# Kernel optimization log

Measured on AMD Instinct MI355X. Metric: run time of the kernel, lower is better.

Reference implementation:

```python
import jax, jax.numpy as jnp
import numpy as np

W_M = 1.0
SIGMA_BASE = 1.0
NUM_GROUPS = 2
NUM_CLASSES = 10
EPS = 1e-12
N, D = 4096, 512


def setup_inputs() -> dict:
    key = jax.random.key(0)
    k1, k2, k3, k4 = jax.random.split(key, 4)
    return {
        "f_s": jax.random.normal(k1, (N, D), dtype=jnp.float32),
        "f_t": jax.random.normal(k2, (N, D), dtype=jnp.float32),
        "groups": jax.random.randint(k3, (N,), 0, NUM_GROUPS),
        "labels": jax.random.randint(k4, (N,), 0, NUM_CLASSES),
    }


def _sqdist(e1, e2):
    # clamped squared euclidean pairwise distances [n1, n2]
    d = (jnp.sum(e1 * e1, axis=1)[:, None]
         + jnp.sum(e2 * e2, axis=1)[None, :]
         - 2.0 * (e1 @ e2.T))
    return jnp.maximum(d, EPS)


def reference(f_s, f_t, groups, labels):
    student = f_s.reshape(f_s.shape[0], -1)
    teacher = f_t.reshape(f_t.shape[0], -1)
    n = student.shape[0]

    D_TS = _sqdist(teacher, student)
    # sigma_avg computed under no_grad over the full teacher-vs-student pdist
    sigma_avg = jax.lax.stop_gradient(jnp.mean(D_TS))
    scale = 2.0 * SIGMA_BASE * sigma_avg

    K_TS = jnp.exp(-D_TS / scale)                      # [N, N]
    K_SS = jnp.exp(-_sqdist(student, student) / scale)  # [N, N]
    K_TT = jnp.exp(-_sqdist(teacher, teacher) / scale)  # [N, N]

    dt = student.dtype
    L = (labels[:, None] == jnp.arange(NUM_CLASSES)[None, :]).astype(dt)   # [N, C]
    Gm = (groups[:, None] == jnp.arange(NUM_GROUPS)[None, :]).astype(dt)   # [N, G]
    S = (L[:, :, None] * Gm[:, None, :]).reshape(n, NUM_CLASSES * NUM_GROUPS)  # [N, CG]

    n_t = L.sum(axis=0)                                 # [C]
    n_s = S.sum(axis=0).reshape(NUM_CLASSES, NUM_GROUPS)  # [C, G]

    # masked pair sums via two small matmuls each
    num_TT = jnp.einsum('nc,nc->c', L, K_TT @ L)                       # [C]
    num_SS = jnp.einsum('np,np->p', S, K_SS @ S).reshape(NUM_CLASSES, NUM_GROUPS)
    A_TS = (K_TS @ S).reshape(n, NUM_CLASSES, NUM_GROUPS)              # [N, C, G]
    num_TS = jnp.einsum('nc,ncg->cg', L, A_TS)                          # [C, G]

    safe_nt = jnp.maximum(n_t, 1.0)
    safe_ns = jnp.maximum(n_s, 1.0)
    mean_TT = num_TT / (safe_nt * safe_nt)              # [C]
    mean_SS = num_SS / (safe_ns * safe_ns)              # [C, G]
    mean_TS = num_TS / (safe_nt[:, None] * safe_ns)     # [C, G]

    valid = (n_t[:, None] > 0) & (n_s > 0)
    term = jnp.where(valid, mean_TT[:, None] + mean_SS - 2.0 * mean_TS, 0.0)
    return 0.5 * W_M * jnp.sum(term)
```

## Files before the change

kernel.cpp:

```cpp
#include <hip/hip_runtime.h>
#include <math.h>

#define NN 4096
#define DD 512
#define NC 10
#define NG 2

#define BM 128
#define BN 128
#define BK 32
#define NT (DD / BK)

#define TSLOT 512
#define SSLOT 256
#define TROWS (NC * TSLOT)
#define SROWS (NC * NG * SSLOT)
#define NTILES 320

typedef __bf16 bf16x8 __attribute__((ext_vector_type(8)));
typedef __bf16 bf16x4 __attribute__((ext_vector_type(4)));
typedef float f32x4 __attribute__((ext_vector_type(4)));

__device__ __forceinline__ void load_lds16(const __bf16* g, __bf16* l) {
    __builtin_amdgcn_global_load_lds((const __attribute__((address_space(1))) void*)g,
                                     (__attribute__((address_space(3))) void*)l, 16, 0, 0);
}

__global__ __launch_bounds__(1024) void k_sortcol(
    const int* __restrict__ labels, const int* __restrict__ groups,
    const float* __restrict__ ft, const float* __restrict__ fs,
    int* __restrict__ perm_t, int* __restrict__ perm_s,
    float* __restrict__ cnts, float* __restrict__ psum, float* __restrict__ ssq) {

    __shared__ int wtot[16][32];
    __shared__ int woff[16][32];
    __shared__ float redsq[4];

    int tid = threadIdx.x;

    if (blockIdx.x < 64) {
        if (tid >= 256) return;
        int b = blockIdx.x;
        int w = tid >> 6, lane = tid & 63;
        const float* srcm = (b < 32) ? ft : fs;
        int r0 = (b & 31) * 128;
        int c0 = tid, c1 = tid + 256;
        float a0 = 0.0f, a1 = 0.0f, sq = 0.0f;
        for (int rw = r0; rw < r0 + 128; ++rw) {
            float v0 = srcm[(size_t)rw * DD + c0];
            float v1 = srcm[(size_t)rw * DD + c1];
            a0 += v0; a1 += v1;
            sq += v0 * v0 + v1 * v1;
        }
        psum[(size_t)b * 512 + c0] = a0;
        psum[(size_t)b * 512 + c1] = a1;
#pragma unroll
        for (int o = 32; o; o >>= 1) sq += __shfl_xor(sq, o);
        if (lane == 0) redsq[w] = sq;
        __syncthreads();
        if (tid == 0) ssq[b] = redsq[0] + redsq[1] + redsq[2] + redsq[3];
        return;
    }

    int lane = tid & 63, w = tid >> 6;

    int4 lab = ((const int4*)labels)[tid];
    int4 grp = ((const int4*)groups)[tid];
    int l[4] = {lab.x, lab.y, lab.z, lab.w};
    int g[4] = {grp.x, grp.y, grp.z, grp.w};

    int cT[NC] = {}, cS[NC * NG] = {};
#pragma unroll
    for (int k = 0; k < 4; ++k) {
        int sb = 2 * l[k] + g[k];
#pragma unroll
        for (int c = 0; c < NC; ++c) cT[c] += (l[k] == c) ? 1 : 0;
#pragma unroll
        for (int c = 0; c < NC * NG; ++c) cS[c] += (sb == c) ? 1 : 0;
    }

    int eT[NC], eS[NC * NG];
#pragma unroll
    for (int c = 0; c < NC; ++c) {
        int x = cT[c];
#pragma unroll
        for (int o = 1; o < 64; o <<= 1) { int v = __shfl_up(x, o); if (lane >= o) x += v; }
        eT[c] = x - cT[c];
        if (lane == 63) wtot[w][c] = x;
    }
#pragma unroll
    for (int c = 0; c < NC * NG; ++c) {
        int x = cS[c];
#pragma unroll
        for (int o = 1; o < 64; o <<= 1) { int v = __shfl_up(x, o); if (lane >= o) x += v; }
        eS[c] = x - cS[c];
        if (lane == 63) wtot[w][NC + c] = x;
    }
    __syncthreads();

    if (tid < NC + NC * NG) {
        int run = 0;
        for (int ww = 0; ww < 16; ++ww) { woff[ww][tid] = run; run += wtot[ww][tid]; }
        int slot = (tid < NC) ? TSLOT : SSLOT;
        cnts[tid] = (float)((run < slot) ? run : slot);
    }
    __syncthreads();

    int runT[NC] = {}, runS[NC * NG] = {};
#pragma unroll
    for (int k = 0; k < 4; ++k) {
        int row = tid * 4 + k;
        int lb = l[k], sb = 2 * l[k] + g[k];
#pragma unroll
        for (int c = 0; c < NC; ++c)
            if (lb == c) {
                int rank = woff[w][c] + eT[c] + runT[c];
                if (rank < TSLOT) perm_t[c * TSLOT + rank] = row;
                runT[c]++;
            }
#pragma unroll
        for (int c = 0; c < NC * NG; ++c)
            if (sb == c) {
                int rank = woff[w][NC + c] + eS[c] + runS[c];
                if (rank < SSLOT) perm_s[c * SSLOT + rank] = row;
                runS[c]++;
            }
    }
}

__global__ void k_prep(const float* __restrict__ ft, const float* __restrict__ fs,
                       const int* __restrict__ perm_t, const int* __restrict__ perm_s,
                       __bf16* __restrict__ Tp, __bf16* __restrict__ Sp,
                       float* __restrict__ ntp, float* __restrict__ nsp,
                       const float* __restrict__ cnts,
                       const float* __restrict__ psum, const float* __restrict__ ssq,
                       float* __restrict__ gbkt, float* __restrict__ invscale) {
    int tid = threadIdx.x;
    if (blockIdx.x == 0 && tid < 64) gbkt[tid] = 0.0f;

    int w = tid >> 6, lane = tid & 63;
    int r = blockIdx.x * 4 + w;
    bool isT = r < TROWS;
    int rr = isT ? r : r - TROWS;
    int c  = isT ? (rr >> 9) : (rr >> 8);
    int j  = isT ? (rr & 511) : (rr & 255);
    int n  = (int)cnts[isT ? c : 10 + c];
    bool valid = j < n;
    int src = valid ? (isT ? perm_t[c * TSLOT + j] : perm_s[c * SSLOT + j]) : 0;
    const float* sp = (isT ? ft : fs) + (size_t)src * DD;
    __bf16* dp = (isT ? Tp : Sp) + (size_t)rr * DD;
    float s = 0.0f;
#pragma unroll
    for (int q = 0; q < 2; ++q) {
        float4 v;
        if (valid) v = ((const float4*)sp)[lane + 64 * q];
        else { v.x = 0.0f; v.y = 0.0f; v.z = 0.0f; v.w = 0.0f; }
        s += v.x * v.x + v.y * v.y + v.z * v.z + v.w * v.w;
        bf16x4 b4;
        b4[0] = (__bf16)v.x; b4[1] = (__bf16)v.y; b4[2] = (__bf16)v.z; b4[3] = (__bf16)v.w;
        *(bf16x4*)(dp + (lane + 64 * q) * 4) = b4;
    }
#pragma unroll
    for (int o = 32; o; o >>= 1) s += __shfl_xor(s, o);
    if (lane == 0) (isT ? ntp : nsp)[rr] = s;

    if (blockIdx.x != 1) return;
    __shared__ float red[8];
    float ssum = (tid < 64) ? ssq[tid] : 0.0f;
    float d = 0.0f;
    for (int col = tid; col < DD; col += 256) {
        float su = 0.0f, sv = 0.0f;
#pragma unroll
        for (int p = 0; p < 32; ++p) {
            su += psum[(size_t)p * 512 + col];
            sv += psum[(size_t)(p + 32) * 512 + col];
        }
        d += su * sv;
    }
#pragma unroll
    for (int o = 32; o; o >>= 1) { ssum += __shfl_xor(ssum, o); d += __shfl_xor(d, o); }
    if (lane == 0) { red[w] = ssum; red[w + 4] = d; }
    __syncthreads();
    if (tid == 0) {
        float S  = red[0] + red[1] + red[2] + red[3];
        float Dt = red[4] + red[5] + red[6] + red[7];
        float sigma = S / (float)NN - 2.0f * Dt / ((float)NN * (float)NN);
        invscale[0] = 1.0f / (2.0f * sigma);
    }
}

__global__ __launch_bounds__(256, 3) void k_gram_all(
    const __bf16* __restrict__ Tp, const __bf16* __restrict__ Sp,
    const float* __restrict__ ntp, const float* __restrict__ nsp,
    const float* __restrict__ cnts,
    const float* __restrict__ invscale_p, float* __restrict__ gbkt) {

    __shared__ __bf16 As[3][4 * 128 * 8];
    __shared__ __bf16 Bs[3][4 * 128 * 8];
    __shared__ float wred[4];

    int swz = ((int)blockIdx.x & 7) * 40 + ((int)blockIdx.x >> 3);
    int mode, bkt, diag, tiv, tjv;
    const __bf16 *A, *B;
    const float *nA, *nB;
    int nrow, ncol;

    if (swz < 100) {
        mode = 0;
        int c = swz / 10, k = swz % 10;
        int ti = 0;
        while (k >= 4 - ti) { k -= 4 - ti; ++ti; }
        int tj = ti + k;
        bkt = c; diag = (ti == tj); tiv = ti; tjv = tj;
        int rb = c * TSLOT + ti * 128, cb = c * TSLOT + tj * 128;
        A = Tp + (size_t)rb * DD; B = Tp + (size_t)cb * DD;
        nA = ntp + rb; nB = ntp + cb;
        int cntc = (int)cnts[c];
        nrow = cntc - ti * 128; ncol = cntc - tj * 128;
    } else if (swz < 160) {
        mode = 1;
        int q = swz - 100;
        int b = q / 3, k = q % 3;
        int ti = (k == 2) ? 1 : 0;
        int tj = (k == 0) ? 0 : 1;
        bkt = 10 + b; diag = (ti == tj); tiv = ti; tjv = tj;
        int rb = b * SSLOT + ti * 128, cb = b * SSLOT + tj * 128;
        A = Sp + (size_t)rb * DD; B = Sp + (size_t)cb * DD;
        nA = nsp + rb; nB = nsp + cb;
        int cntb = (int)cnts[10 + b];
        nrow = cntb - ti * 128; ncol = cntb - tj * 128;
    } else {
        mode = 2;
        int q = swz - 160;
        int c = q >> 4; q &= 15;
        int ti = q >> 2, sj = q & 3;
        int g = sj >> 1, st = sj & 1;
        bkt = 30 + 2 * c + g; diag = 0; tiv = 0; tjv = 0;
        int rb = c * TSLOT + ti * 128;
        int cb = (2 * c + g) * SSLOT + st * 128;
        A = Tp + (size_t)rb * DD; B = Sp + (size_t)cb * DD;
        nA = ntp + rb; nB = nsp + cb;
        nrow = (int)cnts[c] - ti * 128;
        ncol = (int)cnts[10 + 2 * c + g] - st * 128;
    }
    nrow = (nrow < 0) ? 0 : ((nrow > 128) ? 128 : nrow);
    ncol = (ncol < 0) ? 0 : ((ncol > 128) ? 128 : ncol);

    int tid = threadIdx.x;
    int lane = tid & 63, wid = tid >> 6;
    int wr = wid >> 1, wc = wid & 1;
    int l15 = lane & 15, l4 = lane >> 4;

    int ra = tid & 127;
    int qa = tid >> 7;
    const __bf16* gA = A + (size_t)ra * DD + qa * 8;
    const __bf16* gB = B + (size_t)ra * DD + qa * 8;

    f32x4 acc[4][4] = {};

#define STAGE(bb, tt)                                                          \
    do {                                                                       \
        int _k0 = (tt) * BK;                                                   \
        load_lds16(gA + _k0,      &As[(bb)][(size_t)tid * 8]);                 \
        load_lds16(gA + _k0 + 16, &As[(bb)][(size_t)(tid + 256) * 8]);         \
        load_lds16(gB + _k0,      &Bs[(bb)][(size_t)tid * 8]);                 \
        load_lds16(gB + _k0 + 16, &Bs[(bb)][(size_t)(tid + 256) * 8]);         \
    } while (0)

    STAGE(0, 0);
    STAGE(1, 1);
    asm volatile("s_waitcnt vmcnt(4)" ::: "memory");
    __builtin_amdgcn_s_barrier();
    __builtin_amdgcn_sched_barrier(0);

#pragma unroll
    for (int t = 0; t < NT; ++t) {
        int b = t % 3;
        bf16x8 af[4], bfr[4];
#pragma unroll
        for (int im = 0; im < 4; ++im)
            af[im] = *(const bf16x8*)&As[b][((size_t)l4 * 128 + wr * 64 + im * 16 + l15) * 8];
#pragma unroll
        for (int in = 0; in < 4; ++in)
            bfr[in] = *(const bf16x8*)&Bs[b][((size_t)l4 * 128 + wc * 64 + in * 16 + l15) * 8];
        if (t + 2 < NT) STAGE((t + 2) % 3, t + 2);
#pragma unroll
        for (int im = 0; im < 4; ++im)
#pragma unroll
            for (int in = 0; in < 4; ++in)
                acc[im][in] = __builtin_amdgcn_mfma_f32_16x16x32_bf16(af[im], bfr[in], acc[im][in], 0, 0, 0);
        if (t + 1 < NT) {
            if (t + 2 < NT) asm volatile("s_waitcnt vmcnt(4)" ::: "memory");
            else            asm volatile("s_waitcnt vmcnt(0)" ::: "memory");
            __builtin_amdgcn_s_barrier();
            __builtin_amdgcn_sched_barrier(0);
        }
    }
#undef STAGE

    float inv_scale = invscale_p[0];
    float nBv[4];
#pragma unroll
    for (int in = 0; in < 4; ++in)
        nBv[in] = nB[wc * 64 + in * 16 + l15];
    float ssum = 0.0f;
#pragma unroll
    for (int im = 0; im < 4; ++im) {
#pragma unroll
        for (int j = 0; j < 4; ++j) {
            int rl = wr * 64 + im * 16 + l4 * 4 + j;
            float ni = nA[rl];
#pragma unroll
            for (int in = 0; in < 4; ++in) {
                int cl_ = wc * 64 + in * 16 + l15;
                float d = ni + nBv[in] - 2.0f * acc[im][in][j];
                d = fmaxf(d, 1e-12f);
                float kv = __expf(-d * inv_scale);
                bool v = (rl < nrow) && (cl_ < ncol);
                if (mode == 2) {
                    ssum += v ? kv : 0.0f;
                } else {
                    int rg = tiv * 128 + rl, cg = tjv * 128 + cl_;
                    float wgt = !v ? 0.0f
                              : (diag ? (cg > rg ? 2.0f : (cg == rg ? 1.0f : 0.0f))
                                      : 2.0f);
                    ssum += wgt * kv;
                }
            }
        }
    }
#pragma unroll
    for (int o = 1; o < 64; o <<= 1) ssum += __shfl_xor(ssum, o);
    if (lane == 0) wred[wid] = ssum;
    __syncthreads();
    if (tid == 0) atomicAdd(&gbkt[bkt], wred[0] + wred[1] + wred[2] + wred[3]);
}

__global__ void k_out(const float* __restrict__ cnts, const float* __restrict__ gbkt,
                      float* __restrict__ out) {
    __shared__ float sh[80];
    int tid = threadIdx.x;
    if (tid < 30) sh[tid] = cnts[tid];
    else if (tid < 80) sh[tid] = gbkt[tid - 30];
    __syncthreads();
    if (tid == 0) {
        float total = 0.0f;
        for (int c = 0; c < NC; ++c) {
            float ntc = sh[c];
            float sn = fmaxf(ntc, 1.0f);
            float meanTT = sh[30 + c] / (sn * sn);
            for (int g = 0; g < NG; ++g) {
                float nsg = sh[10 + 2 * c + g];
                float ss = fmaxf(nsg, 1.0f);
                float meanSS = sh[40 + 2 * c + g] / (ss * ss);
                float meanTS = sh[60 + 2 * c + g] / (sn * ss);
                if (ntc > 0.0f && nsg > 0.0f)
                    total += meanTT + meanSS - 2.0f * meanTS;
            }
        }
        out[0] = 0.5f * total;
    }
}

extern "C" void kernel_launch(void* const* d_in, const int* in_sizes, int n_in,
                              void* d_out, int out_size, void* d_ws, size_t ws_size,
                              hipStream_t stream) {
    const float* fs     = (const float*)d_in[0];
    const float* ft     = (const float*)d_in[1];
    const int*   groups = (const int*)d_in[2];
    const int*   labels = (const int*)d_in[3];

    __bf16* Tp = (__bf16*)d_ws;
    __bf16* Sp = (__bf16*)d_ws + (size_t)TROWS * DD;
    float* wsf  = (float*)((char*)d_ws + (size_t)(TROWS + SROWS) * DD * sizeof(__bf16));
    float* ntp  = wsf;
    float* nsp  = wsf + 5120;
    float* gbkt = wsf + 10240;
    float* invs = wsf + 10304;
    float* ssq  = wsf + 10306;
    float* cnts = wsf + 10370;
    int* perm_t = (int*)(wsf + 10400);
    int* perm_s = (int*)(wsf + 15520);
    float* psum = wsf + 20640;

    k_sortcol<<<65, 1024, 0, stream>>>(labels, groups, ft, fs,
                                       perm_t, perm_s, cnts, psum, ssq);
    k_prep<<<2560, 256, 0, stream>>>(ft, fs, perm_t, perm_s, Tp, Sp, ntp, nsp,
                                     cnts, psum, ssq, gbkt, invs);
    k_gram_all<<<NTILES, 256, 0, stream>>>(Tp, Sp, ntp, nsp, cnts, invs, gbkt);
    k_out<<<1, 128, 0, stream>>>(cnts, gbkt, (float*)d_out);
}
```

Baseline: 60.04 us.

## Use 256x128 gram tiles with 512-thread blocks to cut tile count

Enlarges the gram-kernel tile from 128x128 to 256x128 using 8 waves per block, reducing the grid from 320 to 180 tiles. Each B tile is now reused across twice as many rows, and the tile enumeration for the symmetric TT/SS buckets is reworked, with the triangular weighting applied uniformly. The cost is that more upper-triangle work inside diagonal blocks is computed and discarded, and fewer blocks may leave compute units idle on a 256-CU part.

Measured after the change: 58.64 us. 1.02x faster.

```diff
diff --git a/kernel.cpp b/kernel.cpp
--- a/kernel.cpp
+++ b/kernel.cpp
@@ -6,7 +6,7 @@
 #define NC 10
 #define NG 2
 
-#define BM 128
+#define BM 256
 #define BN 128
 #define BK 32
 #define NT (DD / BK)
@@ -15,7 +15,7 @@
 #define SSLOT 256
 #define TROWS (NC * TSLOT)
 #define SROWS (NC * NG * SSLOT)
-#define NTILES 320
+#define NTILES 180
 
 typedef __bf16 bf16x8 __attribute__((ext_vector_type(8)));
 typedef __bf16 bf16x4 __attribute__((ext_vector_type(4)));
@@ -189,61 +189,60 @@
     }
 }
 
-__global__ __launch_bounds__(256, 3) void k_gram_all(
+__global__ __launch_bounds__(512, 2) void k_gram_all(
     const __bf16* __restrict__ Tp, const __bf16* __restrict__ Sp,
     const float* __restrict__ ntp, const float* __restrict__ nsp,
     const float* __restrict__ cnts,
     const float* __restrict__ invscale_p, float* __restrict__ gbkt) {
 
-    __shared__ __bf16 As[3][4 * 128 * 8];
+    __shared__ __bf16 As[3][4 * 256 * 8];
     __shared__ __bf16 Bs[3][4 * 128 * 8];
-    __shared__ float wred[4];
-
-    int swz = ((int)blockIdx.x & 7) * 40 + ((int)blockIdx.x >> 3);
-    int mode, bkt, diag, tiv, tjv;
+    __shared__ float wred[8];
+
+    int swz = (int)blockIdx.x;
+    int mode, bkt, ti, tj;
     const __bf16 *A, *B;
     const float *nA, *nB;
     int nrow, ncol;
 
-    if (swz < 100) {
+    if (swz < 60) {
         mode = 0;
-        int c = swz / 10, k = swz % 10;
-        int ti = 0;
-        while (k >= 4 - ti) { k -= 4 - ti; ++ti; }
-        int tj = ti + k;
-        bkt = c; diag = (ti == tj); tiv = ti; tjv = tj;
-        int rb = c * TSLOT + ti * 128, cb = c * TSLOT + tj * 128;
+        int c = swz / 6, r6 = swz % 6;
+        ti = (r6 >= 4) ? 1 : 0;
+        tj = (r6 < 4) ? r6 : (r6 - 2);
+        bkt = c;
+        int rb = c * TSLOT + ti * 256, cb = c * TSLOT + tj * 128;
         A = Tp + (size_t)rb * DD; B = Tp + (size_t)cb * DD;
         nA = ntp + rb; nB = ntp + cb;
         int cntc = (int)cnts[c];
-        nrow = cntc - ti * 128; ncol = cntc - tj * 128;
-    } else if (swz < 160) {
+        nrow = cntc - ti * 256; ncol = cntc - tj * 128;
+    } else if (swz < 100) {
         mode = 1;
-        int q = swz - 100;
-        int b = q / 3, k = q % 3;
-        int ti = (k == 2) ? 1 : 0;
-        int tj = (k == 0) ? 0 : 1;
-        bkt = 10 + b; diag = (ti == tj); tiv = ti; tjv = tj;
-        int rb = b * SSLOT + ti * 128, cb = b * SSLOT + tj * 128;
+        int q = swz - 60;
+        int b = q >> 1;
+        ti = 0; tj = q & 1;
+        bkt = 10 + b;
+        int rb = b * SSLOT, cb = b * SSLOT + tj * 128;
         A = Sp + (size_t)rb * DD; B = Sp + (size_t)cb * DD;
         nA = nsp + rb; nB = nsp + cb;
         int cntb = (int)cnts[10 + b];
-        nrow = cntb - ti * 128; ncol = cntb - tj * 128;
+        nrow = cntb; ncol = cntb - tj * 128;
     } else {
         mode = 2;
-        int q = swz - 160;
-        int c = q >> 4; q &= 15;
-        int ti = q >> 2, sj = q & 3;
-        int g = sj >> 1, st = sj & 1;
-        bkt = 30 + 2 * c + g; diag = 0; tiv = 0; tjv = 0;
-        int rb = c * TSLOT + ti * 128;
+        int q = swz - 100;
+        int c = q >> 3, rem = q & 7;
+        ti = rem >> 2;
+        int g = (rem >> 1) & 1, st = rem & 1;
+        tj = 0;
+        bkt = 30 + 2 * c + g;
+        int rb = c * TSLOT + ti * 256;
         int cb = (2 * c + g) * SSLOT + st * 128;
         A = Tp + (size_t)rb * DD; B = Sp + (size_t)cb * DD;
         nA = ntp + rb; nB = nsp + cb;
-        nrow = (int)cnts[c] - ti * 128;
+        nrow = (int)cnts[c] - ti * 256;
         ncol = (int)cnts[10 + 2 * c + g] - st * 128;
     }
-    nrow = (nrow < 0) ? 0 : ((nrow > 128) ? 128 : nrow);
+    nrow = (nrow < 0) ? 0 : ((nrow > 256) ? 256 : nrow);
     ncol = (ncol < 0) ? 0 : ((ncol > 128) ? 128 : ncol);
 
     int tid = threadIdx.x;
@@ -251,10 +250,8 @@
     int wr = wid >> 1, wc = wid & 1;
     int l15 = lane & 15, l4 = lane >> 4;
 
-    int ra = tid & 127;
-    int qa = tid >> 7;
-    const __bf16* gA = A + (size_t)ra * DD + qa * 8;
-    const __bf16* gB = B + (size_t)ra * DD + qa * 8;
+    const __bf16* gA = A + (size_t)(tid & 255) * DD + (tid >> 8) * 8;
+    const __bf16* gB = B + (size_t)(tid & 127) * DD + (tid >> 7) * 8;
 
     f32x4 acc[4][4] = {};
 
@@ -262,14 +259,13 @@
     do {                                                                       \
         int _k0 = (tt) * BK;                                                   \
         load_lds16(gA + _k0,      &As[(bb)][(size_t)tid * 8]);                 \
-        load_lds16(gA + _k0 + 16, &As[(bb)][(size_t)(tid + 256) * 8]);         \
+        load_lds16(gA + _k0 + 16, &As[(bb)][(size_t)(tid + 512) * 8]);         \
         load_lds16(gB + _k0,      &Bs[(bb)][(size_t)tid * 8]);                 \
-        load_lds16(gB + _k0 + 16, &Bs[(bb)][(size_t)(tid + 256) * 8]);         \
     } while (0)
 
     STAGE(0, 0);
     STAGE(1, 1);
-    asm volatile("s_waitcnt vmcnt(4)" ::: "memory");
+    asm volatile("s_waitcnt vmcnt(3)" ::: "memory");
     __builtin_amdgcn_s_barrier();
     __builtin_amdgcn_sched_barrier(0);
 
@@ -279,7 +275,7 @@
         bf16x8 af[4], bfr[4];
 #pragma unroll
         for (int im = 0; im < 4; ++im)
-            af[im] = *(const bf16x8*)&As[b][((size_t)l4 * 128 + wr * 64 + im * 16 + l15) * 8];
+            af[im] = *(const bf16x8*)&As[b][((size_t)l4 * 256 + wr * 64 + im * 16 + l15) * 8];
 #pragma unroll
         for (int in = 0; in < 4; ++in)
             bfr[in] = *(const bf16x8*)&Bs[b][((size_t)l4 * 128 + wc * 64 + in * 16 + l15) * 8];
@@ -290,7 +286,7 @@
             for (int in = 0; in < 4; ++in)
                 acc[im][in] = __builtin_amdgcn_mfma_f32_16x16x32_bf16(af[im], bfr[in], acc[im][in], 0, 0, 0);
         if (t + 1 < NT) {
-            if (t + 2 < NT) asm volatile("s_waitcnt vmcnt(4)" ::: "memory");
+            if (t + 2 < NT) asm volatile("s_waitcnt vmcnt(3)" ::: "memory");
             else            asm volatile("s_waitcnt vmcnt(0)" ::: "memory");
             __builtin_amdgcn_s_barrier();
             __builtin_amdgcn_sched_barrier(0);
@@ -320,10 +316,9 @@
                 if (mode == 2) {
                     ssum += v ? kv : 0.0f;
                 } else {
-                    int rg = tiv * 128 + rl, cg = tjv * 128 + cl_;
+                    int rg = ti * 256 + rl, cg = tj * 128 + cl_;
                     float wgt = !v ? 0.0f
-                              : (diag ? (cg > rg ? 2.0f : (cg == rg ? 1.0f : 0.0f))
-                                      : 2.0f);
+                              : (cg > rg ? 2.0f : (cg == rg ? 1.0f : 0.0f));
                     ssum += wgt * kv;
                 }
             }
@@ -333,7 +328,12 @@
     for (int o = 1; o < 64; o <<= 1) ssum += __shfl_xor(ssum, o);
     if (lane == 0) wred[wid] = ssum;
     __syncthreads();
-    if (tid == 0) atomicAdd(&gbkt[bkt], wred[0] + wred[1] + wred[2] + wred[3]);
+    if (tid == 0) {
+        float tot = 0.0f;
+#pragma unroll
+        for (int ww = 0; ww < 8; ++ww) tot += wred[ww];
+        atomicAdd(&gbkt[bkt], tot);
+    }
 }
 
 __global__ void k_out(const float* __restrict__ cnts, const float* __restrict__ gbkt,
@@ -387,6 +387,6 @@
                                        perm_t, perm_s, cnts, psum, ssq);
     k_prep<<<2560, 256, 0, stream>>>(ft, fs, perm_t, perm_s, Tp, Sp, ntp, nsp,
                                      cnts, psum, ssq, gbkt, invs);
-    k_gram_all<<<NTILES, 256, 0, stream>>>(Tp, Sp, ntp, nsp, cnts, invs, gbkt);
+    k_gram_all<<<NTILES, 512, 0, stream>>>(Tp, Sp, ntp, nsp, cnts, invs, gbkt);
     k_out<<<1, 128, 0, stream>>>(cnts, gbkt, (float*)d_out);
 }
```
